# Kernel tuning notes

Hardware: AMD Instinct MI355X
Metric: run time of the kernel (lower is better)

The kernel has to match this reference:

```python
import jax, jax.numpy as jnp
import numpy as np

E = 1024   # embed_dim
H = 16     # num_heads
D = E // H # head_dim = 64
Q = 4      # num_queries
B = 4
S = 2048


def setup_inputs() -> dict:
    key = jax.random.key(0)
    ks = jax.random.split(key, 9)
    s = 0.02  # init scale for weights
    return {
        "x":  jax.random.normal(ks[0], (B, S, E), jnp.float32),
        "Wq": jax.random.normal(ks[1], (Q, E, E), jnp.float32) * s,  # stacked per-query Linear weights (torch layout: out,in)
        "bq": jax.random.normal(ks[2], (Q, E), jnp.float32) * s,
        "Wk": jax.random.normal(ks[3], (E, E), jnp.float32) * s,
        "bk": jax.random.normal(ks[4], (E,), jnp.float32) * s,
        "Wv": jax.random.normal(ks[5], (E, E), jnp.float32) * s,
        "bv": jax.random.normal(ks[6], (E,), jnp.float32) * s,
        "Wo": jax.random.normal(ks[7], (E, E), jnp.float32) * s,
        "bo": jax.random.normal(ks[8], (E,), jnp.float32) * s,
    }


def reference(x, Wq, bq, Wk, bk, Wv, bv, Wo, bo):
    B_, S_, E_ = x.shape
    scale = 1.0 / jnp.sqrt(jnp.asarray(D, x.dtype))
    # all query projections at once: (Q,B,S,E) -> (Q,B,S,H,D)
    q = (jnp.einsum('bse,qfe->qbsf', x, Wq) + bq[:, None, None, :]).reshape(Q, B_, S_, H, D)
    k = (x @ Wk.T + bk).reshape(B_, S_, H, D)
    v = (x @ Wv.T + bv).reshape(B_, S_, H, D)
    # NOTE: faithful to the torch code, which never moves the head axis before matmul:
    # scores[q,b,s,h,g] = sum_d q[q,b,s,h,d] * k[b,s,g,d]  -> softmax over heads g
    scores = jnp.einsum('qbshd,bsgd->qbshg', q, k) * scale      # (Q,B,S,H,H)
    probs = jax.nn.softmax(scores, axis=-1)
    out = jnp.einsum('qbshg,bsgd->qbshd', probs, v)             # (Q,B,S,H,D)
    # torch: .transpose(1,2).contiguous().view(B,S,E) == permute to (B,H,S,D) then reshape
    out = jnp.transpose(out, (0, 1, 3, 2, 4)).reshape(Q, B_, S_, E_)
    out = out.sum(axis=0)
    return out @ Wo.T + bo
```

## Files before the change

### kernel.cpp

```cpp
#include <hip/hip_runtime.h>


typedef __bf16 bf16x8 __attribute__((ext_vector_type(8)));
typedef float f32x4 __attribute__((ext_vector_type(4)));
typedef float f32x16 __attribute__((ext_vector_type(16)));

__device__ __forceinline__ unsigned short f2b(float f) {
  unsigned u = __float_as_uint(f);
  return (unsigned short)((u + 0x7fffu + ((u >> 16) & 1u)) >> 16);
}

__device__ __forceinline__ void async16(const void* g, void* l) {
  __builtin_amdgcn_global_load_lds(
      (const __attribute__((address_space(1))) void*)g,
      (__attribute__((address_space(3))) void*)l, 16, 0, 0);
}

__global__ __launch_bounds__(256) void cvt_all(
    const float* __restrict__ x, const float* __restrict__ Wq, const float* __restrict__ Wk,
    const float* __restrict__ Wv, const float* __restrict__ Wo, const float* __restrict__ bq,
    const float* __restrict__ bk, const float* __restrict__ bv,
    unsigned short* __restrict__ xb, unsigned short* __restrict__ wcat,
    unsigned short* __restrict__ wo_b, float* __restrict__ biascat) {
  if (blockIdx.x >= 15360) {
    int j = (blockIdx.x - 15360) * 256 + threadIdx.x;
    if (j < 6144) {
      float v = (j < 4096) ? bq[j] : (j < 5120 ? bk[j - 4096] : bv[j - 5120]);
      biascat[j] = v;
    }
    return;
  }
  int i = blockIdx.x * 256 + threadIdx.x;
  const float* s;
  unsigned short* d;
  int off;
  if (i < 2097152)      { s = x;  d = xb;             off = i; }
  else if (i < 3145728) { s = Wq; d = wcat;           off = i - 2097152; }
  else if (i < 3407872) { s = Wk; d = wcat + 4194304; off = i - 3145728; }
  else if (i < 3670016) { s = Wv; d = wcat + 5242880; off = i - 3407872; }
  else                  { s = Wo; d = wo_b;           off = i - 3670016; }
  float4 v = ((const float4*)s)[off];
  uint2 o;
  o.x = (unsigned)f2b(v.x) | ((unsigned)f2b(v.y) << 16);
  o.y = (unsigned)f2b(v.z) | ((unsigned)f2b(v.w) << 16);
  ((uint2*)d)[off] = o;
}

__global__ __launch_bounds__(512, 2) void gemm256(
    const unsigned short* __restrict__ A, const unsigned short* __restrict__ Bt,
    const float* __restrict__ bias, unsigned short* __restrict__ C,
    int M, int N, int K) {
  __shared__ __align__(16) unsigned short As[4][8192];
  __shared__ __align__(16) unsigned short Bs[4][8192];
  const int t = threadIdx.x;
  const int lane = t & 63, w = t >> 6;
  const int l31 = lane & 31, lhi = lane >> 5;
  const int wm = (w >> 2) * 128, wn = (w & 3) * 64;
  const int bm0 = blockIdx.y * 256, bn0 = blockIdx.x * 256;

  const int rA = t >> 2;
  const int gA = ((t & 3) ^ (rA & 3)) * 8;
  const unsigned short* aS = A + (size_t)(bm0 + rA) * K + gA;
  const unsigned short* bS = Bt + (size_t)(bn0 + rA) * K + gA;
  const size_t rowK128 = (size_t)128 * K;
  const int d0 = t * 8, d1 = d0 + 4096;

  const int swz = l31 & 3;
  const int kc0 = (lhi ^ swz) * 8;
  const int kc1 = ((2 + lhi) ^ swz) * 8;
  int roA[4], roB[2];
#pragma unroll
  for (int mi = 0; mi < 4; ++mi) roA[mi] = (wm + mi * 32 + l31) * 32;
#pragma unroll
  for (int nj = 0; nj < 2; ++nj) roB[nj] = (wn + nj * 32 + l31) * 32;

  f32x16 acc[4][2];
#pragma unroll
  for (int mi = 0; mi < 4; ++mi)
#pragma unroll
    for (int nj = 0; nj < 2; ++nj)
#pragma unroll
      for (int e = 0; e < 16; ++e) acc[mi][nj][e] = 0.f;

#define STG_A(kt_) do { const int b_ = (kt_) & 3; const int ko_ = (kt_) * 32; \
    async16(aS + ko_, &As[b_][d0]); async16(aS + rowK128 + ko_, &As[b_][d1]); } while (0)
#define STG_B(kt_) do { const int b_ = (kt_) & 3; const int ko_ = (kt_) * 32; \
    async16(bS + ko_, &Bs[b_][d0]); async16(bS + rowK128 + ko_, &Bs[b_][d1]); } while (0)

  const int NT = K >> 5;
  STG_A(0); STG_B(0); STG_A(1); STG_B(1);
  asm volatile("s_waitcnt vmcnt(4)" ::: "memory");
  asm volatile("s_barrier" ::: "memory");

  for (int kt = 0; kt < NT; ++kt) {
    const int bi = kt & 3;
    const unsigned short* as_ = As[bi];
    const unsigned short* bs_ = Bs[bi];

    bf16x8 a0[2][2], bb[2][2];
#pragma unroll
    for (int mi = 0; mi < 2; ++mi) {
      a0[mi][0] = *(const bf16x8*)(as_ + roA[mi] + kc0);
      a0[mi][1] = *(const bf16x8*)(as_ + roA[mi] + kc1);
    }
#pragma unroll
    for (int nj = 0; nj < 2; ++nj) {
      bb[nj][0] = *(const bf16x8*)(bs_ + roB[nj] + kc0);
      bb[nj][1] = *(const bf16x8*)(bs_ + roB[nj] + kc1);
    }
    if (kt + 2 < NT) { STG_A(kt + 2); }
    asm volatile("s_barrier" ::: "memory");
    __builtin_amdgcn_s_setprio(1);
#pragma unroll
    for (int mi = 0; mi < 2; ++mi)
#pragma unroll
      for (int nj = 0; nj < 2; ++nj) {
        acc[mi][nj] = __builtin_amdgcn_mfma_f32_32x32x16_bf16(a0[mi][0], bb[nj][0], acc[mi][nj], 0, 0, 0);
        acc[mi][nj] = __builtin_amdgcn_mfma_f32_32x32x16_bf16(a0[mi][1], bb[nj][1], acc[mi][nj], 0, 0, 0);
      }
    __builtin_amdgcn_s_setprio(0);
    asm volatile("s_barrier" ::: "memory");

    bf16x8 a1[2][2];
#pragma unroll
    for (int mi = 0; mi < 2; ++mi) {
      a1[mi][0] = *(const bf16x8*)(as_ + roA[2 + mi] + kc0);
      a1[mi][1] = *(const bf16x8*)(as_ + roA[2 + mi] + kc1);
    }
    if (kt + 2 < NT) { STG_B(kt + 2); }
    asm volatile("s_barrier" ::: "memory");
    __builtin_amdgcn_s_setprio(1);
#pragma unroll
    for (int mi = 0; mi < 2; ++mi)
#pragma unroll
      for (int nj = 0; nj < 2; ++nj) {
        acc[2 + mi][nj] = __builtin_amdgcn_mfma_f32_32x32x16_bf16(a1[mi][0], bb[nj][0], acc[2 + mi][nj], 0, 0, 0);
        acc[2 + mi][nj] = __builtin_amdgcn_mfma_f32_32x32x16_bf16(a1[mi][1], bb[nj][1], acc[2 + mi][nj], 0, 0, 0);
      }
    __builtin_amdgcn_s_setprio(0);
    if (kt + 2 < NT) {
      asm volatile("s_waitcnt vmcnt(4)" ::: "memory");
    } else if (kt + 1 < NT) {
      asm volatile("s_waitcnt vmcnt(0)" ::: "memory");
    }
    asm volatile("s_barrier" ::: "memory");
  }
#undef STG_A
#undef STG_B

#pragma unroll
  for (int mi = 0; mi < 4; ++mi) {
#pragma unroll
    for (int nj = 0; nj < 2; ++nj) {
      int gc = bn0 + wn + nj * 32 + l31;
      float bsv = bias[gc];
#pragma unroll
      for (int reg = 0; reg < 16; ++reg) {
        int gr = bm0 + wm + mi * 32 + (reg & 3) + 8 * (reg >> 2) + 4 * lhi;
        C[(size_t)gr * N + gc] = f2b(acc[mi][nj][reg] + bsv);
      }
    }
  }
}

template <typename OutT>
__global__ __launch_bounds__(256) void gemm_bt(const unsigned short* __restrict__ A,
                                               const unsigned short* __restrict__ Bt,
                                               const float* __restrict__ bias,
                                               OutT* __restrict__ C, int M, int N, int K) {
  __shared__ __align__(16) unsigned short As[128 * 64];
  __shared__ __align__(16) unsigned short Bs[128 * 64];
  const int t = threadIdx.x;
  const int lane = t & 63, w = t >> 6;
  const int wm = (w >> 1) * 64, wn = (w & 1) * 64;
  const int l31 = lane & 31, lhi = lane >> 5;
  const int bm0 = blockIdx.y * 128, bn0 = blockIdx.x * 128;

  f32x16 acc[2][2];
#pragma unroll
  for (int i = 0; i < 2; ++i)
#pragma unroll
    for (int j = 0; j < 2; ++j)
#pragma unroll
      for (int e = 0; e < 16; ++e) acc[i][j][e] = 0.f;

  const int swz = l31 & 7;
  const int qoff = 2 * ((l31 >> 4) & 1);

  for (int k0 = 0; k0 < K; k0 += 64) {
    __syncthreads();
#pragma unroll
    for (int j = 0; j < 4; ++j) {
      int slot = j * 256 + t;
      int r = slot >> 3;
      int p = slot & 7;
      int c = (((p ^ (r & 7)) - 2 * ((r >> 4) & 1)) & 7) * 8;
      async16(A + (size_t)(bm0 + r) * K + k0 + c, As + slot * 8);
      async16(Bt + (size_t)(bn0 + r) * K + k0 + c, Bs + slot * 8);
    }
    __syncthreads();
#pragma unroll
    for (int kk = 0; kk < 64; kk += 16) {
      const int kg = kk >> 3;
      const int pg = ((((kg + lhi + qoff) & 7) ^ swz) << 3);
      bf16x8 af[2], bfr[2];
#pragma unroll
      for (int i = 0; i < 2; ++i)
        af[i] = *(const bf16x8*)(As + (wm + i * 32 + l31) * 64 + pg);
#pragma unroll
      for (int j = 0; j < 2; ++j)
        bfr[j] = *(const bf16x8*)(Bs + (wn + j * 32 + l31) * 64 + pg);
#pragma unroll
      for (int i = 0; i < 2; ++i)
#pragma unroll
        for (int j = 0; j < 2; ++j)
          acc[i][j] = __builtin_amdgcn_mfma_f32_32x32x16_bf16(af[i], bfr[j], acc[i][j], 0, 0, 0);
    }
  }

#pragma unroll
  for (int i = 0; i < 2; ++i) {
#pragma unroll
    for (int j = 0; j < 2; ++j) {
      int gc = bn0 + wn + j * 32 + l31;
      float bsv = bias[gc];
#pragma unroll
      for (int reg = 0; reg < 16; ++reg) {
        int gr = bm0 + wm + i * 32 + (reg & 3) + 8 * (reg >> 2) + 4 * lhi;
        float vv = acc[i][j][reg] + bsv;
        if constexpr (sizeof(OutT) == 2)
          C[(size_t)gr * N + gc] = (OutT)f2b(vv);
        else
          C[(size_t)gr * N + gc] = vv;
      }
    }
  }
}

__global__ __launch_bounds__(256) void attn_scatter(const unsigned short* __restrict__ qkv,
                                                    unsigned short* __restrict__ t) {
  __shared__ __align__(16) unsigned short vs[4][1024];
  __shared__ float ps[4][16 * 17];
  const int w = threadIdx.x >> 6, lane = threadIdx.x & 63;
  const int pos = blockIdx.x * 4 + w;
  const int b = pos >> 11, s = pos & 2047;
  const unsigned short* row = qkv + (size_t)pos * 6144;
  unsigned short* vw = vs[w];
  float* pw = ps[w];
  const int lr = lane & 15, lq = lane >> 4;

  {
    const uint4* sv = (const uint4*)(row + 5120);
    uint4* dv = (uint4*)vw;
    dv[lane * 2] = sv[lane * 2];
    dv[lane * 2 + 1] = sv[lane * 2 + 1];
  }
  bf16x8 kf0 = *(const bf16x8*)(row + 4096 + lr * 64 + lq * 8);
  bf16x8 kf1 = *(const bf16x8*)(row + 4096 + lr * 64 + 32 + lq * 8);

  bf16x8 vf[4];
#pragma unroll
  for (int dc = 0; dc < 4; ++dc) {
#pragma unroll
    for (int j = 0; j < 8; ++j) vf[dc][j] = (__bf16)0.0f;
    if (lq < 2) {
      const __bf16* vb = (const __bf16*)vw;
#pragma unroll
      for (int j = 0; j < 8; ++j)
        vf[dc][j] = vb[(lq * 8 + j) * 64 + dc * 16 + lr];
    }
  }

  f32x4 acc[4];
#pragma unroll
  for (int dc = 0; dc < 4; ++dc) acc[dc] = (f32x4){0.f, 0.f, 0.f, 0.f};

#pragma unroll
  for (int qi = 0; qi < 4; ++qi) {
    bf16x8 qf0 = *(const bf16x8*)(row + qi * 1024 + lr * 64 + lq * 8);
    bf16x8 qf1 = *(const bf16x8*)(row + qi * 1024 + lr * 64 + 32 + lq * 8);
    f32x4 sc = {0.f, 0.f, 0.f, 0.f};
    sc = __builtin_amdgcn_mfma_f32_16x16x32_bf16(qf0, kf0, sc, 0, 0, 0);
    sc = __builtin_amdgcn_mfma_f32_16x16x32_bf16(qf1, kf1, sc, 0, 0, 0);
#pragma unroll
    for (int r = 0; r < 4; ++r) {
      float e = __expf(sc[r] * 0.125f);
      float sum = e;
#pragma unroll
      for (int d = 1; d < 16; d <<= 1) sum += __shfl_xor(sum, d);
      pw[(lq * 4 + r) * 17 + lr] = e / sum;
    }
    bf16x8 pf;
#pragma unroll
    for (int j = 0; j < 8; ++j) pf[j] = (__bf16)0.0f;
    if (lq < 2) {
#pragma unroll
      for (int j = 0; j < 8; ++j) pf[j] = (__bf16)pw[lr * 17 + lq * 8 + j];
    }
#pragma unroll
    for (int dc = 0; dc < 4; ++dc)
      acc[dc] = __builtin_amdgcn_mfma_f32_16x16x32_bf16(vf[dc], pf, acc[dc], 0, 0, 0);
  }

  size_t base = ((size_t)(b * 2048 + 128 * lr + (s >> 4))) * 1024 + 64 * (s & 15) + lq * 4;
#pragma unroll
  for (int dc = 0; dc < 4; ++dc) {
    uint2 u;
    u.x = (unsigned)f2b(acc[dc][0]) | ((unsigned)f2b(acc[dc][1]) << 16);
    u.y = (unsigned)f2b(acc[dc][2]) | ((unsigned)f2b(acc[dc][3]) << 16);
    *(uint2*)(t + base + dc * 16) = u;
  }
}

extern "C" void kernel_launch(void* const* d_in, const int* in_sizes, int n_in,
                              void* d_out, int out_size, void* d_ws, size_t ws_size,
                              hipStream_t stream) {
  const float* x  = (const float*)d_in[0];
  const float* Wq = (const float*)d_in[1];
  const float* bq = (const float*)d_in[2];
  const float* Wk = (const float*)d_in[3];
  const float* bk = (const float*)d_in[4];
  const float* Wv = (const float*)d_in[5];
  const float* bv = (const float*)d_in[6];
  const float* Wo = (const float*)d_in[7];
  const float* bo = (const float*)d_in[8];
  float* out = (float*)d_out;

  char* ws = (char*)d_ws;
  unsigned short* xb      = (unsigned short*)(ws + 0);
  unsigned short* wcat    = (unsigned short*)(ws + 16777216);
  unsigned short* wo_b    = (unsigned short*)(ws + 29360128);
  float*          biascat = (float*)(ws + 31457280);
  unsigned short* qkv     = (unsigned short*)(ws + 31481856);
  unsigned short* t       = xb;

  cvt_all<<<15384, 256, 0, stream>>>(x, Wq, Wk, Wv, Wo, bq, bk, bv, xb, wcat, wo_b, biascat);

  gemm256<<<dim3(24, 32), 512, 0, stream>>>(xb, wcat, biascat, qkv, 8192, 6144, 1024);
  attn_scatter<<<2048, 256, 0, stream>>>(qkv, t);
  gemm_bt<float><<<dim3(8, 64), 256, 0, stream>>>(t, wo_b, bo, out, 8192, 1024, 1024);
}
```

Baseline: 291.3 us.

## Pair rows in LDS tiles and split MFMA phases by k-half

Changes the LDS staging layout of the GEMM so each 128-byte LDS row holds two consecutive matrix rows, with an 8-way XOR swizzle on 16-byte chunks. The compute loop is also reorganised: each phase now loads all four A fragments and both B fragments for one k-half and issues all eight MFMAs, instead of splitting by M sub-tile. The aim is fewer LDS bank conflicts on the fragment reads and a more even MFMA split between the two phases. In exchange, more fragment registers are live per phase and the global-load address pattern becomes less regular.

```diff
diff --git a/kernel.cpp b/kernel.cpp
--- a/kernel.cpp
+++ b/kernel.cpp
@@ -58,21 +58,26 @@
   const int wm = (w >> 2) * 128, wn = (w & 3) * 64;
   const int bm0 = blockIdx.y * 256, bn0 = blockIdx.x * 256;
 
-  const int rA = t >> 2;
-  const int gA = ((t & 3) ^ (rA & 3)) * 8;
-  const unsigned short* aS = A + (size_t)(bm0 + rA) * K + gA;
-  const unsigned short* bS = Bt + (size_t)(bn0 + rA) * K + gA;
-  const size_t rowK128 = (size_t)128 * K;
+  {
+  }
+  const int p0 = t & 7, pr0 = t >> 3;
+  const int u0 = p0 ^ (pr0 & 7);
+  const size_t aoff0 = (size_t)(2 * pr0 + (u0 & 1)) * K + (u0 >> 1) * 8;
+  const unsigned short* aS0 = A + (size_t)bm0 * K + aoff0;
+  const unsigned short* aS1 = aS0 + (size_t)128 * K;
+  const unsigned short* bS0 = Bt + (size_t)bn0 * K + aoff0;
+  const unsigned short* bS1 = bS0 + (size_t)128 * K;
   const int d0 = t * 8, d1 = d0 + 4096;
 
-  const int swz = l31 & 3;
-  const int kc0 = (lhi ^ swz) * 8;
-  const int kc1 = ((2 + lhi) ^ swz) * 8;
-  int roA[4], roB[2];
-#pragma unroll
-  for (int mi = 0; mi < 4; ++mi) roA[mi] = (wm + mi * 32 + l31) * 32;
-#pragma unroll
-  for (int nj = 0; nj < 2; ++nj) roB[nj] = (wn + nj * 32 + l31) * 32;
+  const int plo = 2 * lhi + (l31 & 1);
+  const int pswz = (l31 >> 1) & 7;
+  const int pg0 = ((0 + plo) ^ pswz) * 8;
+  const int pg1 = ((4 + plo) ^ pswz) * 8;
+  int prA[4], prB[2];
+#pragma unroll
+  for (int mi = 0; mi < 4; ++mi) prA[mi] = ((wm + mi * 32 + l31) >> 1) * 64;
+#pragma unroll
+  for (int nj = 0; nj < 2; ++nj) prB[nj] = ((wn + nj * 32 + l31) >> 1) * 64;
 
   f32x16 acc[4][2];
 #pragma unroll
@@ -83,9 +88,9 @@
       for (int e = 0; e < 16; ++e) acc[mi][nj][e] = 0.f;
 
 #define STG_A(kt_) do { const int b_ = (kt_) & 3; const int ko_ = (kt_) * 32; \
-    async16(aS + ko_, &As[b_][d0]); async16(aS + rowK128 + ko_, &As[b_][d1]); } while (0)
+    async16(aS0 + ko_, &As[b_][d0]); async16(aS1 + ko_, &As[b_][d1]); } while (0)
 #define STG_B(kt_) do { const int b_ = (kt_) & 3; const int ko_ = (kt_) * 32; \
-    async16(bS + ko_, &Bs[b_][d0]); async16(bS + rowK128 + ko_, &Bs[b_][d1]); } while (0)
+    async16(bS0 + ko_, &Bs[b_][d0]); async16(bS1 + ko_, &Bs[b_][d1]); } while (0)
 
   const int NT = K >> 5;
   STG_A(0); STG_B(0); STG_A(1); STG_B(1);
@@ -97,46 +102,35 @@
     const unsigned short* as_ = As[bi];
     const unsigned short* bs_ = Bs[bi];
 
-    bf16x8 a0[2][2], bb[2][2];
-#pragma unroll
-    for (int mi = 0; mi < 2; ++mi) {
-      a0[mi][0] = *(const bf16x8*)(as_ + roA[mi] + kc0);
-      a0[mi][1] = *(const bf16x8*)(as_ + roA[mi] + kc1);
-    }
-#pragma unroll
-    for (int nj = 0; nj < 2; ++nj) {
-      bb[nj][0] = *(const bf16x8*)(bs_ + roB[nj] + kc0);
-      bb[nj][1] = *(const bf16x8*)(bs_ + roB[nj] + kc1);
-    }
+    bf16x8 af0[4], bf0[2];
+#pragma unroll
+    for (int mi = 0; mi < 4; ++mi) af0[mi] = *(const bf16x8*)(as_ + prA[mi] + pg0);
+#pragma unroll
+    for (int nj = 0; nj < 2; ++nj) bf0[nj] = *(const bf16x8*)(bs_ + prB[nj] + pg0);
     if (kt + 2 < NT) { STG_A(kt + 2); }
     asm volatile("s_barrier" ::: "memory");
     __builtin_amdgcn_s_setprio(1);
 #pragma unroll
-    for (int mi = 0; mi < 2; ++mi)
-#pragma unroll
-      for (int nj = 0; nj < 2; ++nj) {
-        acc[mi][nj] = __builtin_amdgcn_mfma_f32_32x32x16_bf16(a0[mi][0], bb[nj][0], acc[mi][nj], 0, 0, 0);
-        acc[mi][nj] = __builtin_amdgcn_mfma_f32_32x32x16_bf16(a0[mi][1], bb[nj][1], acc[mi][nj], 0, 0, 0);
-      }
+    for (int mi = 0; mi < 4; ++mi)
+#pragma unroll
+      for (int nj = 0; nj < 2; ++nj)
+        acc[mi][nj] = __builtin_amdgcn_mfma_f32_32x32x16_bf16(af0[mi], bf0[nj], acc[mi][nj], 0, 0, 0);
     __builtin_amdgcn_s_setprio(0);
     asm volatile("s_barrier" ::: "memory");
 
-    bf16x8 a1[2][2];
-#pragma unroll
-    for (int mi = 0; mi < 2; ++mi) {
-      a1[mi][0] = *(const bf16x8*)(as_ + roA[2 + mi] + kc0);
-      a1[mi][1] = *(const bf16x8*)(as_ + roA[2 + mi] + kc1);
-    }
+    bf16x8 af1[4], bf1[2];
+#pragma unroll
+    for (int mi = 0; mi < 4; ++mi) af1[mi] = *(const bf16x8*)(as_ + prA[mi] + pg1);
+#pragma unroll
+    for (int nj = 0; nj < 2; ++nj) bf1[nj] = *(const bf16x8*)(bs_ + prB[nj] + pg1);
     if (kt + 2 < NT) { STG_B(kt + 2); }
     asm volatile("s_barrier" ::: "memory");
     __builtin_amdgcn_s_setprio(1);
 #pragma unroll
-    for (int mi = 0; mi < 2; ++mi)
-#pragma unroll
-      for (int nj = 0; nj < 2; ++nj) {
-        acc[2 + mi][nj] = __builtin_amdgcn_mfma_f32_32x32x16_bf16(a1[mi][0], bb[nj][0], acc[2 + mi][nj], 0, 0, 0);
-        acc[2 + mi][nj] = __builtin_amdgcn_mfma_f32_32x32x16_bf16(a1[mi][1], bb[nj][1], acc[2 + mi][nj], 0, 0, 0);
-      }
+    for (int mi = 0; mi < 4; ++mi)
+#pragma unroll
+      for (int nj = 0; nj < 2; ++nj)
+        acc[mi][nj] = __builtin_amdgcn_mfma_f32_32x32x16_bf16(af1[mi], bf1[nj], acc[mi][nj], 0, 0, 0);
     __builtin_amdgcn_s_setprio(0);
     if (kt + 2 < NT) {
       asm volatile("s_waitcnt vmcnt(4)" ::: "memory");
```

After: 274.6 us. 1.06x faster.
